# Kernel tuning notes

Measured on AMD Instinct MI355X. Metric: run time of the kernel, lower is better.

## Reference

```python
import jax, jax.numpy as jnp
import numpy as np

N = 100000   # nodes
D = 256      # in_dim == out_dim
R = 4        # num_rel
T = 150000   # triangles per relation
H = 2        # nheads (num_rel >= 2)
DH = D // H
EPS = 1e-5


def _layernorm(x, g, b):
    m = jnp.mean(x, axis=-1, keepdims=True)
    v = jnp.mean((x - m) ** 2, axis=-1, keepdims=True)
    return (x - m) * jax.lax.rsqrt(v + EPS) * g + b


def setup_inputs() -> dict:
    key = jax.random.key(0)
    ks = jax.random.split(key, 24)
    s = 1.0 / np.sqrt(D)
    f32 = jnp.float32
    inp = {}
    inp["x"] = jax.random.normal(ks[0], (N, D), f32)
    inp["triangles"] = jax.random.randint(ks[1], (R, 3, T), 0, N)
    inp["edge_index"] = jax.random.randint(ks[2], (R, 2, 8), 0, N)
    inp["node_W"] = jax.random.normal(ks[3], (R, D, D), f32) * s
    inp["tri_W"] = jax.random.normal(ks[4], (R, D, D), f32) * s
    inp["res_W"] = jax.random.normal(ks[5], (D, D), f32) * s
    inp["gate_W"] = jax.random.normal(ks[6], (D, 2 * D), f32) * (1.0 / np.sqrt(2 * D))
    inp["gate_b"] = jnp.zeros((D,), f32)
    inp["in_W"] = jax.random.normal(ks[7], (3 * D, D), f32) * s
    inp["in_b"] = jnp.zeros((3 * D,), f32)
    inp["out_W"] = jax.random.normal(ks[8], (D, D), f32) * s
    inp["out_b"] = jnp.zeros((D,), f32)
    inp["ln1_g"] = jnp.ones((D,), f32)
    inp["ln1_b"] = jnp.zeros((D,), f32)
    inp["lin1_W"] = jax.random.normal(ks[9], (2 * D, D), f32) * s
    inp["lin1_b"] = jnp.zeros((2 * D,), f32)
    inp["lin2_W"] = jax.random.normal(ks[10], (D, 2 * D), f32) * (1.0 / np.sqrt(2 * D))
    inp["lin2_b"] = jnp.zeros((D,), f32)
    inp["ln2_g"] = jnp.ones((D,), f32)
    inp["ln2_b"] = jnp.zeros((D,), f32)
    return inp


def reference(x, triangles, edge_index, node_W, tri_W, res_W, gate_W, gate_b,
              in_W, in_b, out_W, out_b, ln1_g, ln1_b,
              lin1_W, lin1_b, lin2_W, lin2_b, ln2_g, ln2_b):
    del edge_index  # unused by the original forward
    x_res = x @ res_W.T  # [N, D]
    hs = []
    for r in range(R):  # small fixed relation count
        tri = triangles[r]                                 # [3, T]
        tri_feat = (x[tri] @ node_W[r].T).mean(axis=0)     # [T, D]
        tri_msg = tri_feat @ tri_W[r].T                    # [T, D]
        idx = tri.T.reshape(-1)                            # [3T], triangle-major
        rep = jnp.repeat(tri_msg, 3, axis=0)               # [3T, D]
        ssum = jax.ops.segment_sum(rep, idx, num_segments=N)
        cnt = jax.ops.segment_sum(jnp.ones((3 * T,), x.dtype), idx, num_segments=N)
        node_msg = ssum / jnp.maximum(cnt, 1.0)[:, None]   # scatter_mean
        u = jax.nn.elu(node_msg)                           # dropout = identity (eval)
        a = jax.nn.sigmoid(jnp.concatenate([x, u], axis=1) @ gate_W.T + gate_b)
        hs.append(jnp.tanh(u) * a + x_res * (1.0 - a))
    src = jnp.stack(hs, axis=0)                            # [R, N, D] (seq, batch, d)

    # single post-norm TransformerEncoderLayer over the relation axis
    qkv = src @ in_W.T + in_b                              # [R, N, 3D]
    q, k, v = jnp.split(qkv, 3, axis=-1)
    q = q.reshape(R, N, H, DH)
    k = k.reshape(R, N, H, DH)
    v = v.reshape(R, N, H, DH)
    scores = jnp.einsum('qnhd,knhd->nhqk', q, k) / np.sqrt(DH)
    attn = jax.nn.softmax(scores, axis=-1)
    o = jnp.einsum('nhqk,knhd->qnhd', attn, v).reshape(R, N, D)
    o = o @ out_W.T + out_b
    x1 = _layernorm(src + o, ln1_g, ln1_b)
    ff = jax.nn.gelu(x1 @ lin1_W.T + lin1_b, approximate=False) @ lin2_W.T + lin2_b
    x2 = _layernorm(x1 + ff, ln2_g, ln2_b)
    return x2.mean(axis=0)                                 # [N, D]
```

## Files before the change

### kernel.cpp

```cpp
#include <hip/hip_runtime.h>


#define NNODES 100000
#define NPAD   100096
#define DIM    256
#define NREL   4
#define NTRI   150000

typedef unsigned short ushortT;
typedef __attribute__((ext_vector_type(8)))  short   short8;
typedef __attribute__((ext_vector_type(4)))  float   floatx4;
typedef __attribute__((ext_vector_type(4)))  unsigned short ushort4v;

__device__ __forceinline__ float bf2f(ushortT u) {
    union { unsigned int i; float f; } c; c.i = ((unsigned int)u) << 16; return c.f;
}
__device__ __forceinline__ ushortT f2bf(float f) {
    union { float f; unsigned int i; } c; c.f = f;
    unsigned int x = c.i;
    x += 0x7fffu + ((x >> 16) & 1u);
    return (ushortT)(x >> 16);
}


__global__ void cvt_f32_bf16(const float* __restrict__ in, ushortT* __restrict__ out, int n4) {
    int i = blockIdx.x * blockDim.x + threadIdx.x;
    int stride = gridDim.x * blockDim.x;
    for (; i < n4; i += stride) {
        float4 v = ((const float4*)in)[i];
        ushort4v o; o.x = f2bf(v.x); o.y = f2bf(v.y); o.z = f2bf(v.z); o.w = f2bf(v.w);
        ((ushort4v*)out)[i] = o;
    }
}

__global__ void wcomb_kernel(const float* __restrict__ nodeW, const float* __restrict__ triW,
                             ushortT* __restrict__ wcomb) {
    int idx = blockIdx.x * 256 + threadIdx.x;
    int r = idx >> 16, o = (idx >> 8) & 255, k = idx & 255;
    const float* tw = triW  + ((size_t)r << 16) + o * 256;
    const float* nw = nodeW + ((size_t)r << 16) + k;
    float s = 0.f;
    #pragma unroll 8
    for (int j = 0; j < 256; ++j) s += tw[j] * nw[(size_t)j * 256];
    wcomb[idx] = f2bf(s);
}

__global__ void pack_xg(const float* __restrict__ resW, const float* __restrict__ gateW,
                        ushortT* __restrict__ o) {
    int idx = blockIdx.x * 256 + threadIdx.x;
    int r = idx >> 8, k = idx & 255;
    float v = (r < 256) ? resW[r * 256 + k] : gateW[(size_t)(r - 256) * 512 + k];
    o[idx] = f2bf(v);
}

__global__ void pack_wvo(const float* __restrict__ outW, const float* __restrict__ inW,
                         ushortT* __restrict__ o) {
    int idx = blockIdx.x * 256 + threadIdx.x;
    int r = idx >> 8, k = idx & 255;
    int orow = r & 255, d0 = (r >> 8) * 128;
    float s = 0.f;
    #pragma unroll 8
    for (int j = 0; j < 128; ++j)
        s += outW[orow * 256 + d0 + j] * inW[(size_t)(512 + d0 + j) * 256 + k];
    o[idx] = f2bf(s);
}

__global__ void calc_bvo(const float* __restrict__ outW, const float* __restrict__ in_b,
                         float* __restrict__ bvo) {
    int c = blockIdx.x * 256 + threadIdx.x;
    int orow = c & 255, d0 = (c >> 8) * 128;
    float s = 0.f;
    #pragma unroll 8
    for (int j = 0; j < 128; ++j) s += outW[orow * 256 + d0 + j] * in_b[512 + d0 + j];
    bvo[c] = s;
}


__global__ void k_count4(const int* __restrict__ tri, int* __restrict__ cnt4, int n3) {
    int r = blockIdx.y;
    int i = blockIdx.x * 256 + threadIdx.x;
    if (i < n3) atomicAdd(&cnt4[r * NPAD + tri[(size_t)r * n3 + i]], 1);
}

__global__ void k_scan1(const int* __restrict__ cnt4, int* __restrict__ ptr4,
                        int* __restrict__ bsum4, int n) {
    int r = blockIdx.y;
    const int* cnt = cnt4 + r * NPAD;
    int* ptr = ptr4 + r * NPAD;
    int* bsum = bsum4 + r * 512;
    __shared__ int s[256];
    int i = blockIdx.x * 256 + threadIdx.x;
    int v = (i < n) ? cnt[i] : 0;
    s[threadIdx.x] = v; __syncthreads();
    for (int off = 1; off < 256; off <<= 1) {
        int t = (threadIdx.x >= off) ? s[threadIdx.x - off] : 0;
        __syncthreads();
        s[threadIdx.x] += t;
        __syncthreads();
    }
    if (i < n) ptr[i] = s[threadIdx.x] - v;
    if (threadIdx.x == 255) bsum[blockIdx.x] = s[255];
}

__global__ void k_scan2(const int* __restrict__ bsum4, int* __restrict__ bpre4, int nb) {
    int r = blockIdx.x;
    const int* bsum = bsum4 + r * 512;
    int* bpre = bpre4 + r * 512;
    int lane = threadIdx.x & 63;
    int run = 0;
    for (int c = 0; c < nb; c += 64) {
        int idx = c + lane;
        int v = (idx < nb) ? bsum[idx] : 0;
        int incl = v;
        #pragma unroll
        for (int off = 1; off < 64; off <<= 1) {
            int t = __shfl_up(incl, off, 64);
            if (lane >= off) incl += t;
        }
        if (idx < nb) bpre[idx] = run + incl - v;
        run += __shfl(incl, 63, 64);
    }
}

__global__ void k_scan3(const int* __restrict__ bpre4, int* __restrict__ ptr4,
                        int* __restrict__ cur4, int n) {
    int r = blockIdx.y;
    int i = blockIdx.x * 256 + threadIdx.x;
    if (i < n) {
        int p = ptr4[r * NPAD + i] + bpre4[r * 512 + blockIdx.x];
        ptr4[r * NPAD + i] = p; cur4[r * NPAD + i] = p;
    }
}

__global__ void k_fill4(const int* __restrict__ tri, int* __restrict__ cur4,
                        int* __restrict__ adj4, int n3, int T) {
    int r = blockIdx.y;
    int i = blockIdx.x * 256 + threadIdx.x;
    if (i >= n3) return;
    int node = tri[(size_t)r * n3 + i];
    int t = i; if (t >= 2 * T) t -= 2 * T; else if (t >= T) t -= T;
    int pos = atomicAdd(&cur4[r * NPAD + node], 1);
    adj4[(size_t)r * n3 + pos] = t;
}

__global__ __launch_bounds__(256)
void k_meanx(const int* __restrict__ tri, const ushortT* __restrict__ xb,
             ushortT* __restrict__ mx, int T) {
    int t = blockIdx.x * 4 + (threadIdx.x >> 6);
    if (t >= T) return;
    int lane = threadIdx.x & 63;
    int a = tri[t], b = tri[T + t], c = tri[2 * T + t];
    ushort4v va = *(const ushort4v*)(xb + (size_t)a * DIM + lane * 4);
    ushort4v vb = *(const ushort4v*)(xb + (size_t)b * DIM + lane * 4);
    ushort4v vc = *(const ushort4v*)(xb + (size_t)c * DIM + lane * 4);
    ushort4v o;
    o.x = f2bf((bf2f(va.x) + bf2f(vb.x) + bf2f(vc.x)) * (1.0f / 3.0f));
    o.y = f2bf((bf2f(va.y) + bf2f(vb.y) + bf2f(vc.y)) * (1.0f / 3.0f));
    o.z = f2bf((bf2f(va.z) + bf2f(vb.z) + bf2f(vc.z)) * (1.0f / 3.0f));
    o.w = f2bf((bf2f(va.w) + bf2f(vb.w) + bf2f(vc.w)) * (1.0f / 3.0f));
    *(ushort4v*)(mx + (size_t)t * DIM + lane * 4) = o;
}

__global__ __launch_bounds__(256)
void k_gather(const int* __restrict__ ptr, const int* __restrict__ cnt,
              const int* __restrict__ adj, const ushortT* __restrict__ mx,
              ushortT* __restrict__ accb, int n) {
    int node = blockIdx.x * 4 + (threadIdx.x >> 6);
    if (node >= n) return;
    int lane = threadIdx.x & 63;
    int st = ptr[node], c = cnt[node];
    float a0 = 0.f, a1 = 0.f, a2 = 0.f, a3 = 0.f;
    for (int j = 0; j < c; ++j) {
        int t = adj[st + j];
        ushort4v v = *(const ushort4v*)(mx + (size_t)t * DIM + lane * 4);
        a0 += bf2f(v.x); a1 += bf2f(v.y); a2 += bf2f(v.z); a3 += bf2f(v.w);
    }
    float inv = 1.0f / fmaxf((float)c, 1.0f);
    ushort4v o; o.x = f2bf(a0 * inv); o.y = f2bf(a1 * inv);
    o.z = f2bf(a2 * inv); o.w = f2bf(a3 * inv);
    *(ushort4v*)(accb + (size_t)node * DIM + lane * 4) = o;
}


#define BK 32

__device__ __forceinline__ void async_cp16(char* lds, const char* glb) {
    __builtin_amdgcn_global_load_lds((const __attribute__((address_space(1))) unsigned int*)glb,
                                     (__attribute__((address_space(3))) unsigned int*)lds,
                                     16, 0, 0);
}

enum { M_BF16 = 0, M_ELU = 1, M_GATE = 2, M_QKV = 3, M_RES = 4, M_GELU = 5 };

template <int MODE>
__global__ __launch_bounds__(256)
void gemm_bt(const ushortT* __restrict__ A, int lda, size_t aStrZ,
             const ushortT* __restrict__ W, int ldw, size_t wStrZ,
             int M, int K,
             ushortT* __restrict__ outB, int ldo, size_t oStrZ,
             const float* __restrict__ bias,
             const ushortT* __restrict__ aux1,
             const ushortT* __restrict__ aux2,
             int auxLd,
             const ushortT* __restrict__ resB,
             size_t resStrZ) {
    const size_t zi = blockIdx.z;
    A += zi * aStrZ; W += zi * wStrZ;
    if (outB) outB += zi * oStrZ;
    if (resB) resB += zi * resStrZ;

    __shared__ __align__(16) ushortT As[3][128 * BK];
    __shared__ __align__(16) ushortT Bs[3][128 * BK];
    const int tid  = threadIdx.x;
    const int wave = tid >> 6, lane = tid & 63;
    const int m0 = blockIdx.y * 128;
    const int n0 = blockIdx.x * 128;
    const int wm = (wave >> 1) * 64, wn = (wave & 1) * 64;

    floatx4 acc[4][4];
    #pragma unroll
    for (int i = 0; i < 4; ++i)
        #pragma unroll
        for (int j = 0; j < 4; ++j) acc[i][j] = (floatx4){0.f, 0.f, 0.f, 0.f};

    const int r4  = tid >> 2;
    const int b16 = (tid & 3) * 16;
    const char* Ab = (const char*)A + ((size_t)(m0 + r4) * lda) * 2 + b16;
    const char* Wb = (const char*)W + ((size_t)(n0 + r4) * ldw) * 2 + b16;

    const int kq = (lane >> 4) * 8;
    const int ra = wm + (lane & 15);
    const int rb = wn + (lane & 15);

    auto stage = [&](int buf, int k0) {
        char* Asl = (char*)As + buf * 8192 + wave * 1024;
        char* Bsl = (char*)Bs + buf * 8192 + wave * 1024;
        async_cp16(Asl,        Ab + k0 * 2);
        async_cp16(Asl + 4096, Ab + k0 * 2 + (size_t)64 * lda * 2);
        async_cp16(Bsl,        Wb + k0 * 2);
        async_cp16(Bsl + 4096, Wb + k0 * 2 + (size_t)64 * ldw * 2);
    };
    auto compute = [&](int buf) {
        short8 af[4], bfr[4];
        #pragma unroll
        for (int i = 0; i < 4; ++i) {
            af[i]  = *(const short8*)(&As[buf][(ra + i * 16) * BK + kq]);
            bfr[i] = *(const short8*)(&Bs[buf][(rb + i * 16) * BK + kq]);
        }
        #pragma unroll
        for (int mi = 0; mi < 4; ++mi)
            #pragma unroll
            for (int ni = 0; ni < 4; ++ni)
                acc[mi][ni] = __builtin_amdgcn_mfma_f32_16x16x32_bf16(af[mi], bfr[ni], acc[mi][ni], 0, 0, 0);
    };

    const int NIT = K / BK;
    stage(0, 0);
    stage(1, BK);
    asm volatile("s_waitcnt vmcnt(4)" ::: "memory");
    __builtin_amdgcn_s_barrier();

    int bufc = 0, bufs = 2;
    for (int it = 0; it < NIT; ++it) {
        if (it + 2 < NIT) stage(bufs, (it + 2) * BK);
        compute(bufc);
        if (it + 1 < NIT) {
            if (it + 2 < NIT) asm volatile("s_waitcnt vmcnt(4)" ::: "memory");
            else              asm volatile("s_waitcnt vmcnt(0)" ::: "memory");
            __builtin_amdgcn_s_barrier();
        }
        bufc = (bufc == 2) ? 0 : bufc + 1;
        bufs = (bufs == 2) ? 0 : bufs + 1;
    }

    const int cl = lane & 15, rw = (lane >> 4) * 4;
    #pragma unroll
    for (int mi = 0; mi < 4; ++mi) {
        #pragma unroll
        for (int e = 0; e < 4; ++e) {
            const int m = m0 + wm + mi * 16 + rw + e;
            if (m >= M) continue;
            #pragma unroll
            for (int ni = 0; ni < 4; ++ni) {
                const int col = n0 + wn + ni * 16 + cl;
                float c = acc[mi][ni][e];
                if (MODE == M_BF16) {
                    outB[(size_t)m * ldo + col] = f2bf(c);
                } else if (MODE == M_ELU) {
                    c = c > 0.f ? c : (__expf(c) - 1.0f);
                    outB[(size_t)m * ldo + col] = f2bf(c);
                } else if (MODE == M_GATE) {
                    float g  = bf2f(aux1[(size_t)m * auxLd + col]);
                    float xr = bf2f(aux2[(size_t)m * auxLd + col]);
                    float uv = bf2f(A[(size_t)m * lda + col]);
                    float a  = 1.0f / (1.0f + __expf(-(c + g + bias[col])));
                    float th = 1.0f - 2.0f / (__expf(2.0f * uv) + 1.0f);
                    float h  = th * a + xr * (1.0f - a);
                    outB[(size_t)m * ldo + col] = f2bf(h);
                } else if (MODE == M_QKV) {
                    outB[(size_t)m * ldo + col] = f2bf(c + bias[col]);
                } else if (MODE == M_RES) {
                    outB[(size_t)m * ldo + col] =
                        f2bf(c + bias[col] + bf2f(resB[(size_t)m * 256 + col]));
                } else if (MODE == M_GELU) {
                    float t = c + bias[col];
                    outB[(size_t)m * ldo + col] = f2bf(0.5f * t * (1.0f + erff(t * 0.70710678118f)));
                }
            }
        }
    }
}

__global__ __launch_bounds__(256)
void attn_score(const ushortT* __restrict__ qk, size_t rstride,
                float* __restrict__ Aw, int nvalid) {
    int n = blockIdx.x * 4 + (threadIdx.x >> 6);
    if (n >= nvalid) return;
    int lane = threadIdx.x & 63;
    int head = lane >> 5, hl = lane & 31;
    int d = head * 128 + hl * 4;
    float q[NREL][4], k[NREL][4];
    #pragma unroll
    for (int r = 0; r < NREL; ++r) {
        const ushortT* base = qk + r * rstride + (size_t)n * 512;
        ushort4v qv = *(const ushort4v*)(base + d);
        ushort4v kv = *(const ushort4v*)(base + 256 + d);
        q[r][0] = bf2f(qv.x); q[r][1] = bf2f(qv.y); q[r][2] = bf2f(qv.z); q[r][3] = bf2f(qv.w);
        k[r][0] = bf2f(kv.x); k[r][1] = bf2f(kv.y); k[r][2] = bf2f(kv.z); k[r][3] = bf2f(kv.w);
    }
    float s[NREL][NREL];
    #pragma unroll
    for (int qr = 0; qr < NREL; ++qr)
        #pragma unroll
        for (int kr = 0; kr < NREL; ++kr) {
            float p = q[qr][0] * k[kr][0] + q[qr][1] * k[kr][1] +
                      q[qr][2] * k[kr][2] + q[qr][3] * k[kr][3];
            #pragma unroll
            for (int off = 1; off < 32; off <<= 1) p += __shfl_xor(p, off, 32);
            s[qr][kr] = p * 0.08838834764831845f;
        }
    if (hl < 16) {
        int qr = hl >> 2, kr = hl & 3;
        float mx = fmaxf(fmaxf(s[qr][0], s[qr][1]), fmaxf(s[qr][2], s[qr][3]));
        float e0 = __expf(s[qr][0] - mx), e1 = __expf(s[qr][1] - mx);
        float e2 = __expf(s[qr][2] - mx), e3 = __expf(s[qr][3] - mx);
        float e  = __expf(s[qr][kr] - mx);
        Aw[((size_t)n * 2 + head) * 16 + qr * 4 + kr] = e / (e0 + e1 + e2 + e3);
    }
}

__global__ __launch_bounds__(256)
void attn_combine_ln1(const ushortT* __restrict__ vo4, size_t rstride,
                      const ushortT* __restrict__ h4, size_t hstride,
                      const float* __restrict__ Aw,
                      const float* __restrict__ ob,
                      const float* __restrict__ g, const float* __restrict__ b,
                      ushortT* __restrict__ x1, size_t x1str, int nvalid) {
    int n = blockIdx.x * 4 + (threadIdx.x >> 6);
    if (n >= nvalid) return;
    int lane = threadIdx.x & 63;
    int d4 = lane * 4;
    const float* ap = Aw + (size_t)n * 32;
    float a0[NREL][NREL], a1[NREL][NREL];
    #pragma unroll
    for (int qr = 0; qr < NREL; ++qr)
        #pragma unroll
        for (int kr = 0; kr < NREL; ++kr) {
            a0[qr][kr] = ap[qr * 4 + kr];
            a1[qr][kr] = ap[16 + qr * 4 + kr];
        }
    float vl[NREL][4], vh[NREL][4];
    #pragma unroll
    for (int kr = 0; kr < NREL; ++kr) {
        const ushortT* base = vo4 + kr * rstride + (size_t)n * 512;
        ushort4v lo = *(const ushort4v*)(base + d4);
        ushort4v hi = *(const ushort4v*)(base + 256 + d4);
        vl[kr][0] = bf2f(lo.x); vl[kr][1] = bf2f(lo.y); vl[kr][2] = bf2f(lo.z); vl[kr][3] = bf2f(lo.w);
        vh[kr][0] = bf2f(hi.x); vh[kr][1] = bf2f(hi.y); vh[kr][2] = bf2f(hi.z); vh[kr][3] = bf2f(hi.w);
    }
    float bb0 = ob[d4], bb1 = ob[d4 + 1], bb2 = ob[d4 + 2], bb3 = ob[d4 + 3];
    float g0 = g[d4], g1 = g[d4 + 1], g2 = g[d4 + 2], g3 = g[d4 + 3];
    float e0 = b[d4], e1 = b[d4 + 1], e2 = b[d4 + 2], e3 = b[d4 + 3];
    #pragma unroll
    for (int qr = 0; qr < NREL; ++qr) {
        ushort4v hv = *(const ushort4v*)(h4 + qr * hstride + (size_t)n * 256 + d4);
        float z0 = bf2f(hv.x) + bb0, z1 = bf2f(hv.y) + bb1;
        float z2 = bf2f(hv.z) + bb2, z3 = bf2f(hv.w) + bb3;
        #pragma unroll
        for (int kr = 0; kr < NREL; ++kr) {
            float c0 = a0[qr][kr], c1 = a1[qr][kr];
            z0 += c0 * vl[kr][0] + c1 * vh[kr][0];
            z1 += c0 * vl[kr][1] + c1 * vh[kr][1];
            z2 += c0 * vl[kr][2] + c1 * vh[kr][2];
            z3 += c0 * vl[kr][3] + c1 * vh[kr][3];
        }
        float s = z0 + z1 + z2 + z3;
        #pragma unroll
        for (int off = 1; off < 64; off <<= 1) s += __shfl_xor(s, off, 64);
        float mean = s * (1.0f / 256.0f);
        float dx = z0 - mean, dy = z1 - mean, dz = z2 - mean, dw = z3 - mean;
        float qs = dx * dx + dy * dy + dz * dz + dw * dw;
        #pragma unroll
        for (int off = 1; off < 64; off <<= 1) qs += __shfl_xor(qs, off, 64);
        float rstd = rsqrtf(qs * (1.0f / 256.0f) + 1e-5f);
        ushort4v o;
        o.x = f2bf(dx * rstd * g0 + e0); o.y = f2bf(dy * rstd * g1 + e1);
        o.z = f2bf(dz * rstd * g2 + e2); o.w = f2bf(dw * rstd * g3 + e3);
        *(ushort4v*)(x1 + qr * x1str + (size_t)n * 256 + d4) = o;
    }
}

__global__ __launch_bounds__(256)
void ln2_out(const ushortT* __restrict__ zb, size_t zStrZ,
             const float* __restrict__ g, const float* __restrict__ b,
             float* __restrict__ outc, int n) {
    int row = blockIdx.x * 4 + (threadIdx.x >> 6);
    if (row >= n) return;
    int lane = threadIdx.x & 63, c0 = lane * 4;
    float g0 = g[c0], g1 = g[c0 + 1], g2 = g[c0 + 2], g3 = g[c0 + 3];
    float b0 = b[c0], b1 = b[c0 + 1], b2 = b[c0 + 2], b3 = b[c0 + 3];
    float o0 = 0.f, o1 = 0.f, o2 = 0.f, o3 = 0.f;
    #pragma unroll
    for (int r = 0; r < NREL; ++r) {
        ushort4v v = *(const ushort4v*)(zb + r * zStrZ + (size_t)row * 256 + c0);
        float vx = bf2f(v.x), vy = bf2f(v.y), vz = bf2f(v.z), vw = bf2f(v.w);
        float s = vx + vy + vz + vw;
        #pragma unroll
        for (int off = 1; off < 64; off <<= 1) s += __shfl_xor(s, off, 64);
        float mean = s * (1.0f / 256.0f);
        float dx = vx - mean, dy = vy - mean, dz = vz - mean, dw = vw - mean;
        float qs = dx * dx + dy * dy + dz * dz + dw * dw;
        #pragma unroll
        for (int off = 1; off < 64; off <<= 1) qs += __shfl_xor(qs, off, 64);
        float rstd = rsqrtf(qs * (1.0f / 256.0f) + 1e-5f);
        o0 += 0.25f * (dx * rstd * g0 + b0);
        o1 += 0.25f * (dy * rstd * g1 + b1);
        o2 += 0.25f * (dz * rstd * g2 + b2);
        o3 += 0.25f * (dw * rstd * g3 + b3);
    }
    float4 o; o.x = o0; o.y = o1; o.z = o2; o.w = o3;
    *(float4*)(outc + (size_t)row * 256 + c0) = o;
}


extern "C" void kernel_launch(void* const* d_in, const int* in_sizes, int n_in,
                              void* d_out, int out_size, void* d_ws, size_t ws_size,
                              hipStream_t stream) {
    const float* x      = (const float*)d_in[0];
    const int*   tri    = (const int*)d_in[1];
    const float* nodeW  = (const float*)d_in[3];
    const float* triW   = (const float*)d_in[4];
    const float* resW   = (const float*)d_in[5];
    const float* gateW  = (const float*)d_in[6];
    const float* gate_b = (const float*)d_in[7];
    const float* inW    = (const float*)d_in[8];
    const float* in_b   = (const float*)d_in[9];
    const float* outW   = (const float*)d_in[10];
    const float* out_b  = (const float*)d_in[11];
    const float* ln1g   = (const float*)d_in[12];
    const float* ln1b   = (const float*)d_in[13];
    const float* lin1W  = (const float*)d_in[14];
    const float* lin1b  = (const float*)d_in[15];
    const float* lin2W  = (const float*)d_in[16];
    const float* lin2b  = (const float*)d_in[17];
    const float* ln2g   = (const float*)d_in[18];
    const float* ln2b   = (const float*)d_in[19];
    float* out = (float*)d_out;

    char* ws = (char*)d_ws;
    size_t off = 0;
    auto alloc = [&](size_t bytes) -> char* {
        char* p = ws + off; off += (bytes + 255) & ~(size_t)255; return p;
    };
    ushortT* accAll  = (ushortT*)alloc((size_t)NREL * NPAD * 256 * 2);
    ushortT* xall_b  = (ushortT*)alloc((size_t)NPAD * 256 * 2);
    ushortT* wcomb   = (ushortT*)alloc((size_t)NREL * 65536 * 2);
    ushortT* xgW_b   = (ushortT*)alloc((size_t)131072 * 2);
    ushortT* gateW_b = (ushortT*)alloc((size_t)131072 * 2);
    ushortT* inW_b   = (ushortT*)alloc((size_t)131072 * 2);
    ushortT* wvo_b   = (ushortT*)alloc((size_t)131072 * 2);
    ushortT* lin1_bf = (ushortT*)alloc((size_t)131072 * 2);
    ushortT* lin2_bf = (ushortT*)alloc((size_t)131072 * 2);
    float*   bvo     = (float*)  alloc((size_t)512 * 4);
    size_t persist = off;
    size_t scratch = (ws_size > persist) ? (ws_size - persist) : 0;
    char* S = ws + persist;

    int*     cnt4  = (int*)(S);
    int*     ptr4  = cnt4 + 4 * NPAD;
    int*     cur4  = ptr4 + 4 * NPAD;
    int*     bsum4 = cur4 + 4 * NPAD;
    int*     bpre4 = bsum4 + 4 * 512;
    int*     adj4  = bpre4 + 4 * 512;
    size_t csrBytes = ((char*)(adj4 + (size_t)4 * 3 * NTRI) - S + 255) & ~(size_t)255;
    const size_t mxBytes = (size_t)NTRI * 256 * 2;
    if (scratch < csrBytes + mxBytes + 65536) return;
    ushortT* mxbf = (ushortT*)(S + csrBytes);

    const size_t ROWB = 9344;
    int TT = (NNODES + 127) / 128;
    int tpcMax = (int)(scratch / (ROWB * 128));
    if (tpcMax < 1) return;
    if (tpcMax > TT) tpcMax = TT;
    const int nchunks = (TT + tpcMax - 1) / tpcMax;
    const int tpc = (TT + nchunks - 1) / nchunks;
    const size_t NcPad = (size_t)tpc * 128;

    ushortT* xg   = (ushortT*)(S);
    ushortT* ubf4 = (ushortT*)(S + 1024 * NcPad);
    ushortT* h4   = (ushortT*)(S + 3072 * NcPad);
    ushortT* qk4  = (ushortT*)(S + 5120 * NcPad);
    ushortT* vo4  = qk4;
    ushortT* x1   = (ushortT*)(S);
    ushortT* ffg  = (ushortT*)(S + 2048 * NcPad);
    ushortT* zbb  = (ushortT*)(S + 6144 * NcPad);
    float*   Aw   = (float*)  (S + 9216 * NcPad);

    cvt_f32_bf16<<<2048, 256, 0, stream>>>(x, xall_b, NNODES * 64);
    cvt_f32_bf16<<<64, 256, 0, stream>>>(gateW, gateW_b, 131072 / 4);
    cvt_f32_bf16<<<64, 256, 0, stream>>>(inW,   inW_b,   131072 / 4);
    cvt_f32_bf16<<<64, 256, 0, stream>>>(lin1W, lin1_bf, 131072 / 4);
    cvt_f32_bf16<<<64, 256, 0, stream>>>(lin2W, lin2_bf, 131072 / 4);
    pack_xg<<<512, 256, 0, stream>>>(resW, gateW, xgW_b);
    pack_wvo<<<512, 256, 0, stream>>>(outW, inW, wvo_b);
    calc_bvo<<<2, 256, 0, stream>>>(outW, in_b, bvo);
    wcomb_kernel<<<1024, 256, 0, stream>>>(nodeW, triW, wcomb);

    const int NB = (NNODES + 255) / 256;
    const int N3B = (3 * NTRI + 255) / 256;
    (void)hipMemsetAsync(cnt4, 0, (size_t)4 * NPAD * 4, stream);
    k_count4<<<dim3(N3B, 4), 256, 0, stream>>>(tri, cnt4, 3 * NTRI);
    k_scan1<<<dim3(NB, 4), 256, 0, stream>>>(cnt4, ptr4, bsum4, NNODES);
    k_scan2<<<4, 64, 0, stream>>>(bsum4, bpre4, NB);
    k_scan3<<<dim3(NB, 4), 256, 0, stream>>>(bpre4, ptr4, cur4, NNODES);
    k_fill4<<<dim3(N3B, 4), 256, 0, stream>>>(tri, cur4, adj4, 3 * NTRI, NTRI);
    for (int r = 0; r < NREL; ++r) {
        const int* trir = tri + (size_t)r * 3 * NTRI;
        k_meanx<<<(NTRI + 3) / 4, 256, 0, stream>>>(trir, xall_b, mxbf, NTRI);
        k_gather<<<(NNODES + 3) / 4, 256, 0, stream>>>(
            ptr4 + (size_t)r * NPAD, cnt4 + (size_t)r * NPAD,
            adj4 + (size_t)r * 3 * NTRI, mxbf,
            accAll + (size_t)r * NPAD * 256, NNODES);
    }

    for (int ci = 0; ci < nchunks; ++ci) {
        const int rows0 = ci * tpc * 128;
        int mact = NNODES - rows0;
        if (mact <= 0) break;
        if (mact > tpc * 128) mact = tpc * 128;
        const int tiles = (mact + 127) / 128;
        const dim3 g2z(2, tiles, NREL), g4z(4, tiles, NREL);
        const int nwblk = (mact + 3) / 4;
        float* outc = out + (size_t)rows0 * 256;
        const ushortT* xbf = xall_b + (size_t)rows0 * 256;

        gemm_bt<M_BF16><<<dim3(4, tiles), 256, 0, stream>>>(xbf, 256, 0, xgW_b, 256, 0, mact, 256,
            xg, 512, 0, nullptr, nullptr, nullptr, 0, nullptr, 0);
        gemm_bt<M_ELU><<<g2z, 256, 0, stream>>>(
            accAll + (size_t)rows0 * 256, 256, (size_t)NPAD * 256,
            wcomb, 256, 65536, mact, 256,
            ubf4, 256, 256 * NcPad, nullptr, nullptr, nullptr, 0, nullptr, 0);
        gemm_bt<M_GATE><<<g2z, 256, 0, stream>>>(
            ubf4, 256, 256 * NcPad, gateW_b + 256, 512, 0, mact, 256,
            h4, 256, 256 * NcPad, gate_b, xg + 256, xg, 512, nullptr, 0);
        gemm_bt<M_QKV><<<g4z, 256, 0, stream>>>(
            h4, 256, 256 * NcPad, inW_b, 256, 0, mact, 256,
            qk4, 512, 512 * NcPad, in_b, nullptr, nullptr, 0, nullptr, 0);
        attn_score<<<nwblk, 256, 0, stream>>>(qk4, 512 * NcPad, Aw, mact);
        gemm_bt<M_QKV><<<g4z, 256, 0, stream>>>(
            h4, 256, 256 * NcPad, wvo_b, 256, 0, mact, 256,
            vo4, 512, 512 * NcPad, bvo, nullptr, nullptr, 0, nullptr, 0);
        attn_combine_ln1<<<nwblk, 256, 0, stream>>>(vo4, 512 * NcPad, h4, 256 * NcPad,
            Aw, out_b, ln1g, ln1b, x1, 256 * NcPad, mact);
        gemm_bt<M_GELU><<<g4z, 256, 0, stream>>>(x1, 256, 256 * NcPad, lin1_bf, 256, 0, mact, 256,
            ffg, 512, 512 * NcPad, lin1b, nullptr, nullptr, 0, nullptr, 0);
        gemm_bt<M_RES><<<g2z, 256, 0, stream>>>(ffg, 512, 512 * NcPad, lin2_bf, 512, 0, mact, 512,
            zbb, 256, 256 * NcPad, lin2b, nullptr, nullptr, 0, x1, 256 * NcPad);
        ln2_out<<<nwblk, 256, 0, stream>>>(zbb, 256 * NcPad, ln2g, ln2b, outc, mact);
    }
}
```

Before: 3.247 ms.

## Stage GEMM epilogue through padded LDS for vectorized 16-byte stores and fast erf

```diff
diff --git a/kernel.cpp b/kernel.cpp
--- a/kernel.cpp
+++ b/kernel.cpp
@@ -20,6 +20,14 @@
     unsigned int x = c.i;
     x += 0x7fffu + ((x >> 16) & 1u);
     return (ushortT)(x >> 16);
+}
+__device__ __forceinline__ float erf_as(float x) {
+    float ax = fabsf(x);
+    float k  = 1.0f / (1.0f + 0.3275911f * ax);
+    float p  = k * (0.254829592f + k * (-0.284496736f + k * (1.421413741f +
+               k * (-1.453152027f + k * 1.061405429f))));
+    float r  = 1.0f - p * __expf(-ax * ax);
+    return copysignf(r, x);
 }
 
 
@@ -183,6 +191,7 @@
 
 
 #define BK 32
+#define PADW 133
 
 __device__ __forceinline__ void async_cp16(char* lds, const char* glb) {
     __builtin_amdgcn_global_load_lds((const __attribute__((address_space(1))) unsigned int*)glb,
@@ -209,8 +218,7 @@
     if (outB) outB += zi * oStrZ;
     if (resB) resB += zi * resStrZ;
 
-    __shared__ __align__(16) ushortT As[3][128 * BK];
-    __shared__ __align__(16) ushortT Bs[3][128 * BK];
+    __shared__ __align__(16) char smem[128 * PADW * 4];
     const int tid  = threadIdx.x;
     const int wave = tid >> 6, lane = tid & 63;
     const int m0 = blockIdx.y * 128;
@@ -233,19 +241,21 @@
     const int rb = wn + (lane & 15);
 
     auto stage = [&](int buf, int k0) {
-        char* Asl = (char*)As + buf * 8192 + wave * 1024;
-        char* Bsl = (char*)Bs + buf * 8192 + wave * 1024;
+        char* Asl = smem + buf * 8192 + wave * 1024;
+        char* Bsl = smem + 24576 + buf * 8192 + wave * 1024;
         async_cp16(Asl,        Ab + k0 * 2);
         async_cp16(Asl + 4096, Ab + k0 * 2 + (size_t)64 * lda * 2);
         async_cp16(Bsl,        Wb + k0 * 2);
         async_cp16(Bsl + 4096, Wb + k0 * 2 + (size_t)64 * ldw * 2);
     };
     auto compute = [&](int buf) {
+        const ushortT* Abuf = (const ushortT*)(smem + buf * 8192);
+        const ushortT* Bbuf = (const ushortT*)(smem + 24576 + buf * 8192);
         short8 af[4], bfr[4];
         #pragma unroll
         for (int i = 0; i < 4; ++i) {
-            af[i]  = *(const short8*)(&As[buf][(ra + i * 16) * BK + kq]);
-            bfr[i] = *(const short8*)(&Bs[buf][(rb + i * 16) * BK + kq]);
+            af[i]  = *(const short8*)(Abuf + (ra + i * 16) * BK + kq);
+            bfr[i] = *(const short8*)(Bbuf + (rb + i * 16) * BK + kq);
         }
         #pragma unroll
         for (int mi = 0; mi < 4; ++mi)
@@ -273,40 +283,68 @@
         bufs = (bufs == 2) ? 0 : bufs + 1;
     }
 
+    __syncthreads();
+    float* Ct = (float*)smem;
     const int cl = lane & 15, rw = (lane >> 4) * 4;
     #pragma unroll
-    for (int mi = 0; mi < 4; ++mi) {
-        #pragma unroll
-        for (int e = 0; e < 4; ++e) {
-            const int m = m0 + wm + mi * 16 + rw + e;
-            if (m >= M) continue;
+    for (int mi = 0; mi < 4; ++mi)
+        #pragma unroll
+        for (int ni = 0; ni < 4; ++ni)
             #pragma unroll
-            for (int ni = 0; ni < 4; ++ni) {
-                const int col = n0 + wn + ni * 16 + cl;
-                float c = acc[mi][ni][e];
-                if (MODE == M_BF16) {
-                    outB[(size_t)m * ldo + col] = f2bf(c);
-                } else if (MODE == M_ELU) {
-                    c = c > 0.f ? c : (__expf(c) - 1.0f);
-                    outB[(size_t)m * ldo + col] = f2bf(c);
-                } else if (MODE == M_GATE) {
-                    float g  = bf2f(aux1[(size_t)m * auxLd + col]);
-                    float xr = bf2f(aux2[(size_t)m * auxLd + col]);
-                    float uv = bf2f(A[(size_t)m * lda + col]);
-                    float a  = 1.0f / (1.0f + __expf(-(c + g + bias[col])));
-                    float th = 1.0f - 2.0f / (__expf(2.0f * uv) + 1.0f);
-                    float h  = th * a + xr * (1.0f - a);
-                    outB[(size_t)m * ldo + col] = f2bf(h);
-                } else if (MODE == M_QKV) {
-                    outB[(size_t)m * ldo + col] = f2bf(c + bias[col]);
-                } else if (MODE == M_RES) {
-                    outB[(size_t)m * ldo + col] =
-                        f2bf(c + bias[col] + bf2f(resB[(size_t)m * 256 + col]));
-                } else if (MODE == M_GELU) {
-                    float t = c + bias[col];
-                    outB[(size_t)m * ldo + col] = f2bf(0.5f * t * (1.0f + erff(t * 0.70710678118f)));
+            for (int e = 0; e < 4; ++e)
+                Ct[(wm + mi * 16 + rw + e) * PADW + (wn + ni * 16 + cl)] = acc[mi][ni][e];
+    __syncthreads();
+
+    const int row = tid >> 1;
+    const int cb  = (tid & 1) * 64;
+    const int m   = m0 + row;
+    if (m < M) {
+        #pragma unroll
+        for (int k8 = 0; k8 < 8; ++k8) {
+            const int c0  = cb + k8 * 8;
+            const int col = n0 + c0;
+            float v[8];
+            #pragma unroll
+            for (int j = 0; j < 8; ++j) v[j] = Ct[row * PADW + c0 + j];
+            short8 ov;
+            if (MODE == M_BF16) {
+                #pragma unroll
+                for (int j = 0; j < 8; ++j) ov[j] = (short)f2bf(v[j]);
+            } else if (MODE == M_ELU) {
+                #pragma unroll
+                for (int j = 0; j < 8; ++j) {
+                    float c = v[j] > 0.f ? v[j] : (__expf(v[j]) - 1.0f);
+                    ov[j] = (short)f2bf(c);
+                }
+            } else if (MODE == M_GATE) {
+                short8 gv = *(const short8*)(aux1 + (size_t)m * auxLd + col);
+                short8 xv = *(const short8*)(aux2 + (size_t)m * auxLd + col);
+                short8 uv = *(const short8*)(A + (size_t)m * lda + col);
+                #pragma unroll
+                for (int j = 0; j < 8; ++j) {
+                    float g  = bf2f((ushortT)gv[j]);
+                    float xr = bf2f((ushortT)xv[j]);
+                    float u  = bf2f((ushortT)uv[j]);
+                    float a  = 1.0f / (1.0f + __expf(-(v[j] + g + bias[col + j])));
+                    float th = 1.0f - 2.0f / (__expf(2.0f * u) + 1.0f);
+                    ov[j] = (short)f2bf(th * a + xr * (1.0f - a));
+                }
+            } else if (MODE == M_QKV) {
+                #pragma unroll
+                for (int j = 0; j < 8; ++j) ov[j] = (short)f2bf(v[j] + bias[col + j]);
+            } else if (MODE == M_RES) {
+                short8 rv = *(const short8*)(resB + (size_t)m * 256 + col);
+                #pragma unroll
+                for (int j = 0; j < 8; ++j)
+                    ov[j] = (short)f2bf(v[j] + bias[col + j] + bf2f((ushortT)rv[j]));
+            } else if (MODE == M_GELU) {
+                #pragma unroll
+                for (int j = 0; j < 8; ++j) {
+                    float t = v[j] + bias[col + j];
+                    ov[j] = (short)f2bf(0.5f * t * (1.0f + erf_as(t * 0.70710678118f)));
                 }
             }
+            *(short8*)(&outB[(size_t)m * ldo + col]) = ov;
         }
     }
 }
```

Result: slower. 3.383 ms (+4.2%).
